# Kernel tuning notes

Hardware: AMD Instinct MI355X
Metric: run time of the kernel (lower is better)

## Reference

```python
import jax, jax.numpy as jnp
import numpy as np

EPS = 1e-3
D_MODEL = 512
SEQ = 1024
BATCH = 4
N_LAYERS = 2
N_HEAD = 8
D_HEAD = 64
D_INNER = 1024


def _position_table(n_pos, d):
    # Faithful to PositionEncoding: sin applied to even cols; the cos line in
    # the source is a no-op (missing assignment), so odd cols stay raw.
    j = np.arange(d)
    pos = np.arange(n_pos)[:, None]
    pe = pos / np.power(10000.0, 2 * (j // 2) / d)
    pe[0] = 0.0
    pe[1:, 0::2] = np.sin(pe[1:, 0::2])
    return jnp.asarray(pe, dtype=jnp.float32)


def _layer_norm(z, a, b):
    # torch.std is unbiased (ddof=1); eps added to sigma, not variance
    mu = jnp.mean(z, axis=-1, keepdims=True)
    sigma = jnp.sqrt(jnp.sum((z - mu) ** 2, axis=-1, keepdims=True) / (z.shape[-1] - 1))
    return (z - mu) / (sigma + EPS) * a + b


def setup_inputs() -> dict:
    key = jax.random.key(0)
    ks = jax.random.split(key, 10)
    s = 0.02
    return {
        "x": jax.random.normal(ks[0], (BATCH, SEQ, D_MODEL), dtype=jnp.float32),
        "pos_enc": _position_table(SEQ, D_MODEL),
        "w_qs": jax.random.normal(ks[1], (N_LAYERS, N_HEAD, D_MODEL, D_HEAD), dtype=jnp.float32) * s,
        "w_ks": jax.random.normal(ks[2], (N_LAYERS, N_HEAD, D_MODEL, D_HEAD), dtype=jnp.float32) * s,
        "w_vs": jax.random.normal(ks[3], (N_LAYERS, N_HEAD, D_MODEL, D_HEAD), dtype=jnp.float32) * s,
        "ln1_a": jnp.ones((N_LAYERS, D_MODEL), dtype=jnp.float32),
        "ln1_b": jnp.zeros((N_LAYERS, D_MODEL), dtype=jnp.float32),
        "w1": jax.random.normal(ks[4], (N_LAYERS, D_INNER, D_MODEL), dtype=jnp.float32) * s,
        "b1": jax.random.normal(ks[5], (N_LAYERS, D_INNER), dtype=jnp.float32) * s,
        "w2": jax.random.normal(ks[6], (N_LAYERS, D_MODEL, D_INNER), dtype=jnp.float32) * s,
        "b2": jax.random.normal(ks[7], (N_LAYERS, D_MODEL), dtype=jnp.float32) * s,
        "ln2_a": jnp.ones((N_LAYERS, D_MODEL), dtype=jnp.float32),
        "ln2_b": jnp.zeros((N_LAYERS, D_MODEL), dtype=jnp.float32),
    }


def reference(x, pos_enc, w_qs, w_ks, w_vs, ln1_a, ln1_b, w1, b1, w2, b2, ln2_a, ln2_b):
    temper = jnp.sqrt(jnp.float32(D_MODEL))  # scale uses d_model, not d_k (as in source)
    x = x + pos_enc[None, :, :]
    for i in range(N_LAYERS):
        residual = x
        # per-head projections: [h, b, l, dk]
        q = jnp.einsum('bld,hdk->hblk', x, w_qs[i])
        k = jnp.einsum('bld,hdk->hblk', x, w_ks[i])
        v = jnp.einsum('bld,hdv->hblv', x, w_vs[i])
        attn = jax.nn.softmax(jnp.einsum('hbqk,hbmk->hbqm', q, k) / temper, axis=-1)
        out = jnp.einsum('hbqm,hbmv->hbqv', attn, v)
        # permute(1,2,0,3): concat heads along feature dim -> [b, l, h*dv]
        out = out.transpose(1, 2, 0, 3).reshape(BATCH, SEQ, N_HEAD * D_HEAD)
        x = _layer_norm(out + residual, ln1_a[i], ln1_b[i])
        # positionwise FFN (1x1 convs == linears)
        h = jax.nn.relu(jnp.einsum('bld,fd->blf', x, w1[i]) + b1[i])
        o = jnp.einsum('blf,df->bld', h, w2[i]) + b2[i]
        x = _layer_norm(o + x, ln2_a[i], ln2_b[i])
    return x
```

## Files before the change

kernel.cpp:

```cpp
#include <hip/hip_runtime.h>
#include <math.h>

#define D_MODEL 512
#define SEQ     1024
#define BATCH   4
#define N_LAYERS 2
#define N_HEAD  8
#define D_HEAD  64
#define D_INNER 1024
#define NTOK    (BATCH*SEQ)
#define LN_EPS  1e-3f

typedef float f32x4 __attribute__((ext_vector_type(4)));
typedef short bf16x8 __attribute__((ext_vector_type(8)));
typedef unsigned short ushort_t;
typedef unsigned int uint_t;
typedef unsigned long long ull_t;

__device__ inline ushort_t f2bf(float f) {
    uint_t u = __float_as_uint(f);
    u += 0x7FFFu + ((u >> 16) & 1u);
    return (ushort_t)(u >> 16);
}
__device__ inline float bf2f(ushort_t h) {
    return __uint_as_float((uint_t)h << 16);
}

__device__ __forceinline__ void gload16(const ushort_t* g, ushort_t* l) {
    __builtin_amdgcn_global_load_lds(
        (const __attribute__((address_space(1))) void*)g,
        (__attribute__((address_space(3))) void*)l, 16, 0, 0);
}

#define PREP_E0 (NTOK * D_MODEL)
#define PREP_E1 (1536 * 512)
#define PREP_EW (N_LAYERS * D_INNER * D_MODEL)
#define PREP_TOTAL (PREP_E0 + 2 * PREP_E1 + 2 * PREP_EW)

__global__ void prep_kernel(const float* __restrict__ x,
                            const float* __restrict__ pe,
                            const float* __restrict__ w_qs,
                            const float* __restrict__ w_ks,
                            const float* __restrict__ w_vs,
                            const float* __restrict__ w1,
                            const float* __restrict__ w2,
                            float* __restrict__ X,
                            ushort_t* __restrict__ Xraw,
                            ushort_t* __restrict__ Wqkv,
                            ushort_t* __restrict__ WqkvL,
                            ushort_t* __restrict__ W1b,
                            ushort_t* __restrict__ W2b) {
    int idx = blockIdx.x * 256 + threadIdx.x;
    if (idx < PREP_E0) {
        int l = (idx / D_MODEL) % SEQ;
        int d = idx % D_MODEL;
        float xv = x[idx];
        X[idx] = xv + pe[l * D_MODEL + d];
        Xraw[idx] = f2bf(xv);
        return;
    }
    idx -= PREP_E0;
    if (idx < 2 * PREP_E1) {
        int layer = idx / PREP_E1;
        int j = idx - layer * PREP_E1;
        int n = j >> 9, k = j & 511;
        int which = n >> 9, h = (n >> 6) & 7, d = n & 63;
        size_t wofs = (size_t)layer * N_HEAD * D_MODEL * D_HEAD;
        const float* W = (which == 0) ? w_qs + wofs
                       : (which == 1) ? w_ks + wofs : w_vs + wofs;
        float v = W[((size_t)h * D_MODEL + k) * D_HEAD + d];
        ushort_t hv = f2bf(v);
        Wqkv[(size_t)layer * PREP_E1 + j] = hv;
        if (layer == 0) WqkvL[j] = f2bf(v - bf2f(hv));
        return;
    }
    idx -= 2 * PREP_E1;
    if (idx < PREP_EW) { W1b[idx] = f2bf(w1[idx]); return; }
    idx -= PREP_EW;
    W2b[idx] = f2bf(w2[idx]);
}

__device__ inline void qkv_scatter(f32x4 a, int n, int m_base,
                                   const float* __restrict__ pew,
                                   ushort_t* Qhi, ushort_t* Qlo,
                                   ushort_t* Khi, ushort_t* Klo,
                                   ushort_t* Vt) {
    int which = n >> 9, hd = n & 511;
    int head = hd >> 6, d = hd & 63;
    int hb = head * BATCH + (m_base >> 10);
    int l  = m_base & 1023;
    if (pew) {
#pragma unroll
        for (int r = 0; r < 4; r++) a[r] += pew[(size_t)(l + r) * 1536 + n];
    }
    if (which == 2) {
        ushort4 pk = make_ushort4(f2bf(a[0]), f2bf(a[1]), f2bf(a[2]), f2bf(a[3]));
        *(ushort4*)(Vt + ((size_t)hb * D_HEAD + d) * SEQ + l) = pk;
    } else {
        ushort_t* H = (which == 0) ? Qhi : Khi;
        ushort_t* L = (which == 0) ? Qlo : Klo;
#pragma unroll
        for (int r = 0; r < 4; r++) {
            float v = a[r];
            ushort_t hv = f2bf(v);
            size_t off = ((size_t)hb * SEQ + l + r) * D_HEAD + d;
            H[off] = hv;
            L[off] = f2bf(v - bf2f(hv));
        }
    }
}

template<int MODE, int TM, int TN>
__global__ __launch_bounds__(256, (TM == 128 ? 3 : 4))
void gemm_kernel(const ushort_t* __restrict__ A, const ushort_t* __restrict__ Bt,
                 const float* __restrict__ bias, const float* __restrict__ pew,
                 float* __restrict__ outF, ushort_t* __restrict__ outB,
                 ushort_t* __restrict__ Qhi, ushort_t* __restrict__ Qlo,
                 ushort_t* __restrict__ Khi, ushort_t* __restrict__ Klo,
                 ushort_t* __restrict__ Vt,
                 int M, int N, int K) {
    constexpr int BK = 128;
    constexpr int WM = TM / 2, WN = TN / 2;
    constexpr int MT = WM / 16, NT = WN / 16;
    constexpr int WA = TM / 16;
    constexpr int WB = TN / 16;
    __shared__ ushort_t As[TM * BK];
    __shared__ ushort_t Bs[TN * BK];
    const int tid = threadIdx.x;
    const int m0 = blockIdx.y * TM, n0 = blockIdx.x * TN;
    const int w = tid >> 6, lane = tid & 63;
    const int wr = w >> 1, wc = w & 1;
    const int col = lane & 15, quad = lane >> 4;
    const int srow = lane >> 4;
    const int scc  = lane & 15;

    f32x4 acc[MT][NT] = {};

    for (int k0 = 0; k0 < K; k0 += BK) {
        __syncthreads();
#pragma unroll
        for (int q = 0; q < WA; q++) {
            int row = (w * WA + q) * 4 + srow;
            int sch = scc ^ (row & 7);
            gload16(A + (size_t)(m0 + row) * K + k0 + sch * 8,
                    &As[(w * WA + q) * 4 * BK]);
        }
#pragma unroll
        for (int q = 0; q < WB; q++) {
            int row = (w * WB + q) * 4 + srow;
            int sch = scc ^ (row & 7);
            gload16(Bt + (size_t)(n0 + row) * K + k0 + sch * 8,
                    &Bs[(w * WB + q) * 4 * BK]);
        }
        __syncthreads();
#pragma unroll
        for (int ks = 0; ks < BK; ks += 32) {
            const int cb = ks >> 3;
            const int sc_ = ((cb + quad) ^ (col & 7)) * 8;
            bf16x8 af[MT], bfr[NT];
#pragma unroll
            for (int t = 0; t < MT; t++)
                af[t] = *(const bf16x8*)(&As[(wr * WM + t * 16 + col) * BK + sc_]);
#pragma unroll
            for (int t = 0; t < NT; t++)
                bfr[t] = *(const bf16x8*)(&Bs[(wc * WN + t * 16 + col) * BK + sc_]);
#pragma unroll
            for (int mt = 0; mt < MT; mt++)
#pragma unroll
                for (int nt = 0; nt < NT; nt++)
                    acc[mt][nt] = __builtin_amdgcn_mfma_f32_16x16x32_bf16(
                        af[mt], bfr[nt], acc[mt][nt], 0, 0, 0);
        }
    }

#pragma unroll
    for (int mt = 0; mt < MT; mt++) {
#pragma unroll
        for (int nt = 0; nt < NT; nt++) {
            int n = n0 + wc * WN + nt * 16 + col;
            int m_base = m0 + wr * WM + mt * 16 + quad * 4;
            if (MODE == 0) {
                qkv_scatter(acc[mt][nt], n, m_base, pew, Qhi, Qlo, Khi, Klo, Vt);
            } else {
#pragma unroll
                for (int r = 0; r < 4; r++) {
                    int m = m_base + r;
                    float v = acc[mt][nt][r];
                    if (MODE == 1) {
                        float t = fmaxf(v + bias[n], 0.f);
                        outB[(size_t)m * N + n] = f2bf(t);
                    } else {
                        outF[(size_t)m * N + n] = v + bias[n];
                    }
                }
            }
        }
    }
}

__global__ __launch_bounds__(256, 4)
void gemm_hilo_kernel(const float* __restrict__ A,
                      const ushort_t* __restrict__ Bh,
                      const ushort_t* __restrict__ Bl,
                      float* __restrict__ outF, int M, int N, int K) {
    __shared__ ushort_t Ash[64][72];
    __shared__ ushort_t Asl[64][72];
    __shared__ ushort_t Bsh[64][72];
    __shared__ ushort_t Bsl[64][72];
    const int tid = threadIdx.x;
    const int m0 = blockIdx.y * 64, n0 = blockIdx.x * 64;
    const int w = tid >> 6, lane = tid & 63;
    const int wm = (w >> 1) * 32, wn = (w & 1) * 32;
    const int col = lane & 15, quad = lane >> 4;

    f32x4 acc[2][2] = {};

    for (int k0 = 0; k0 < K; k0 += 64) {
        __syncthreads();
#pragma unroll
        for (int p = 0; p < 4; p++) {
            int idx = p * 256 + tid;
            int row = idx >> 4, c4 = (idx & 15) * 4;
            float4 v = *(const float4*)(A + (size_t)(m0 + row) * K + k0 + c4);
            ushort_t h0 = f2bf(v.x), h1 = f2bf(v.y), h2 = f2bf(v.z), h3 = f2bf(v.w);
            *(ushort4*)(&Ash[row][c4]) = make_ushort4(h0, h1, h2, h3);
            *(ushort4*)(&Asl[row][c4]) = make_ushort4(
                f2bf(v.x - bf2f(h0)), f2bf(v.y - bf2f(h1)),
                f2bf(v.z - bf2f(h2)), f2bf(v.w - bf2f(h3)));
        }
#pragma unroll
        for (int p = 0; p < 2; p++) {
            int idx = p * 256 + tid;
            int row = idx >> 3, ch = (idx & 7) * 8;
            *(uint4*)(&Bsh[row][ch]) =
                *(const uint4*)(Bh + (size_t)(n0 + row) * K + k0 + ch);
            *(uint4*)(&Bsl[row][ch]) =
                *(const uint4*)(Bl + (size_t)(n0 + row) * K + k0 + ch);
        }
        __syncthreads();
#pragma unroll
        for (int ks = 0; ks < 64; ks += 32) {
            bf16x8 ah[2], al[2], bh[2], bl[2];
#pragma unroll
            for (int t = 0; t < 2; t++) {
                ah[t] = *(const bf16x8*)(&Ash[wm + t * 16 + col][ks + quad * 8]);
                al[t] = *(const bf16x8*)(&Asl[wm + t * 16 + col][ks + quad * 8]);
                bh[t] = *(const bf16x8*)(&Bsh[wn + t * 16 + col][ks + quad * 8]);
                bl[t] = *(const bf16x8*)(&Bsl[wn + t * 16 + col][ks + quad * 8]);
            }
#pragma unroll
            for (int mt = 0; mt < 2; mt++)
#pragma unroll
                for (int nt = 0; nt < 2; nt++) {
                    acc[mt][nt] = __builtin_amdgcn_mfma_f32_16x16x32_bf16(
                        ah[mt], bh[nt], acc[mt][nt], 0, 0, 0);
                    acc[mt][nt] = __builtin_amdgcn_mfma_f32_16x16x32_bf16(
                        ah[mt], bl[nt], acc[mt][nt], 0, 0, 0);
                    acc[mt][nt] = __builtin_amdgcn_mfma_f32_16x16x32_bf16(
                        al[mt], bh[nt], acc[mt][nt], 0, 0, 0);
                }
        }
    }

#pragma unroll
    for (int mt = 0; mt < 2; mt++)
#pragma unroll
        for (int nt = 0; nt < 2; nt++) {
            int n = n0 + wn + nt * 16 + col;
#pragma unroll
            for (int r = 0; r < 4; r++) {
                int m = m0 + wm + mt * 16 + quad * 4 + r;
                outF[(size_t)m * N + n] = acc[mt][nt][r];
            }
        }
}

template<bool HILO>
__global__ __launch_bounds__(256, 2)
void attention_kernel(const ushort_t* __restrict__ Qhi,
                      const ushort_t* __restrict__ Qlo,
                      const ushort_t* __restrict__ Khi,
                      const ushort_t* __restrict__ Klo,
                      const ushort_t* __restrict__ Vt,
                      float* __restrict__ P0,
                      float* __restrict__ P1,
                      float2* __restrict__ ML) {
    const int bid = blockIdx.x;
    const int split = bid >> 8;
    const int r8  = bid & 255;
    const int j   = r8 >> 3;
    const int hb  = (r8 & 7) * 4 + (j >> 3);
    const int qp2 = j & 7;
    const int h = hb >> 2, b = hb & 3;
    const int tid = threadIdx.x;
    const int w = tid >> 6, lane = tid & 63;
    const int col = lane & 15, quad = lane >> 4;
    const size_t kbase = (size_t)hb * SEQ * D_HEAD;
    const size_t vbase = (size_t)hb * D_HEAD * SEQ;

    __shared__ ushort_t Kh[64][72];
    __shared__ ushort_t Kl[HILO ? 64 : 1][72];
    __shared__ ushort_t Vs[64][72];
    __shared__ ushort_t Pl[4][2][16][72];

    const int srow0 = tid >> 3;
    const int srow1 = 32 + (tid >> 3);
    const int sch   = (tid & 7) * 8;

    const int qbase = qp2 * 128 + w * 32;
    bf16x8 qh[2][2], ql[2][2];
#pragma unroll
    for (int u = 0; u < 2; u++) {
        const ushort_t* qp = Qhi + kbase + (size_t)(qbase + u * 16 + col) * D_HEAD;
        qh[u][0] = *(const bf16x8*)(qp + quad * 8);
        qh[u][1] = *(const bf16x8*)(qp + 32 + quad * 8);
        if (HILO) {
            const ushort_t* lp = Qlo + kbase + (size_t)(qbase + u * 16 + col) * D_HEAD;
            ql[u][0] = *(const bf16x8*)(lp + quad * 8);
            ql[u][1] = *(const bf16x8*)(lp + 32 + quad * 8);
        }
    }

    f32x4 acco[2][4] = {};
    float mrun[2] = {-1e30f, -1e30f}, lrun[2] = {0.f, 0.f};
    const float inv_temper = 0.04419417382415922f;

    const int tbeg = split * (SEQ / 2);
    const int tend = tbeg + SEQ / 2;

    uint4 rK0, rK1, rL0, rL1, rV0, rV1;
    {
        const int t0 = tbeg;
        rK0 = *(const uint4*)(Khi + kbase + (size_t)(t0 + srow0) * D_HEAD + sch);
        rK1 = *(const uint4*)(Khi + kbase + (size_t)(t0 + srow1) * D_HEAD + sch);
        if (HILO) {
            rL0 = *(const uint4*)(Klo + kbase + (size_t)(t0 + srow0) * D_HEAD + sch);
            rL1 = *(const uint4*)(Klo + kbase + (size_t)(t0 + srow1) * D_HEAD + sch);
        }
        rV0 = *(const uint4*)(Vt + vbase + (size_t)srow0 * SEQ + t0 + sch);
        rV1 = *(const uint4*)(Vt + vbase + (size_t)srow1 * SEQ + t0 + sch);
    }

    for (int t0 = tbeg; t0 < tend; t0 += 64) {
        __syncthreads();
        *(uint4*)(&Kh[srow0][sch]) = rK0;
        *(uint4*)(&Kh[srow1][sch]) = rK1;
        if (HILO) {
            *(uint4*)(&Kl[srow0][sch]) = rL0;
            *(uint4*)(&Kl[srow1][sch]) = rL1;
        }
        *(uint4*)(&Vs[srow0][sch]) = rV0;
        *(uint4*)(&Vs[srow1][sch]) = rV1;
        __syncthreads();

        if (t0 + 64 < tend) {
            const int tn = t0 + 64;
            rK0 = *(const uint4*)(Khi + kbase + (size_t)(tn + srow0) * D_HEAD + sch);
            rK1 = *(const uint4*)(Khi + kbase + (size_t)(tn + srow1) * D_HEAD + sch);
            if (HILO) {
                rL0 = *(const uint4*)(Klo + kbase + (size_t)(tn + srow0) * D_HEAD + sch);
                rL1 = *(const uint4*)(Klo + kbase + (size_t)(tn + srow1) * D_HEAD + sch);
            }
            rV0 = *(const uint4*)(Vt + vbase + (size_t)srow0 * SEQ + tn + sch);
            rV1 = *(const uint4*)(Vt + vbase + (size_t)srow1 * SEQ + tn + sch);
        }

        float sc[2][4][4];
#pragma unroll
        for (int nt = 0; nt < 4; nt++) {
            bf16x8 kh0 = *(const bf16x8*)(&Kh[nt * 16 + col][quad * 8]);
            bf16x8 kh1 = *(const bf16x8*)(&Kh[nt * 16 + col][32 + quad * 8]);
            f32x4 s0 = {}, s1 = {};
            s0 = __builtin_amdgcn_mfma_f32_16x16x32_bf16(kh0, qh[0][0], s0, 0, 0, 0);
            s0 = __builtin_amdgcn_mfma_f32_16x16x32_bf16(kh1, qh[0][1], s0, 0, 0, 0);
            s1 = __builtin_amdgcn_mfma_f32_16x16x32_bf16(kh0, qh[1][0], s1, 0, 0, 0);
            s1 = __builtin_amdgcn_mfma_f32_16x16x32_bf16(kh1, qh[1][1], s1, 0, 0, 0);
            if (HILO) {
                bf16x8 kl0 = *(const bf16x8*)(&Kl[nt * 16 + col][quad * 8]);
                bf16x8 kl1 = *(const bf16x8*)(&Kl[nt * 16 + col][32 + quad * 8]);
                s0 = __builtin_amdgcn_mfma_f32_16x16x32_bf16(kl0, qh[0][0], s0, 0, 0, 0);
                s0 = __builtin_amdgcn_mfma_f32_16x16x32_bf16(kl1, qh[0][1], s0, 0, 0, 0);
                s0 = __builtin_amdgcn_mfma_f32_16x16x32_bf16(kh0, ql[0][0], s0, 0, 0, 0);
                s0 = __builtin_amdgcn_mfma_f32_16x16x32_bf16(kh1, ql[0][1], s0, 0, 0, 0);
                s1 = __builtin_amdgcn_mfma_f32_16x16x32_bf16(kl0, qh[1][0], s1, 0, 0, 0);
                s1 = __builtin_amdgcn_mfma_f32_16x16x32_bf16(kl1, qh[1][1], s1, 0, 0, 0);
                s1 = __builtin_amdgcn_mfma_f32_16x16x32_bf16(kh0, ql[1][0], s1, 0, 0, 0);
                s1 = __builtin_amdgcn_mfma_f32_16x16x32_bf16(kh1, ql[1][1], s1, 0, 0, 0);
            }
#pragma unroll
            for (int r = 0; r < 4; r++) {
                sc[0][nt][r] = s0[r] * inv_temper;
                sc[1][nt][r] = s1[r] * inv_temper;
            }
        }

#pragma unroll
        for (int u = 0; u < 2; u++) {
            float tmax = sc[u][0][0];
#pragma unroll
            for (int nt = 0; nt < 4; nt++)
#pragma unroll
                for (int r = 0; r < 4; r++) tmax = fmaxf(tmax, sc[u][nt][r]);
            tmax = fmaxf(tmax, __shfl_xor(tmax, 16, 64));
            tmax = fmaxf(tmax, __shfl_xor(tmax, 32, 64));

            float mn = fmaxf(mrun[u], tmax);
            float alpha = __expf(mrun[u] - mn);
            mrun[u] = mn;
            float tsum = 0.f;
#pragma unroll
            for (int nt = 0; nt < 4; nt++) {
                float p0 = __expf(sc[u][nt][0] - mn);
                float p1 = __expf(sc[u][nt][1] - mn);
                float p2 = __expf(sc[u][nt][2] - mn);
                float p3 = __expf(sc[u][nt][3] - mn);
                tsum += (p0 + p1) + (p2 + p3);
                ull_t pk = (ull_t)f2bf(p0) | ((ull_t)f2bf(p1) << 16)
                         | ((ull_t)f2bf(p2) << 32) | ((ull_t)f2bf(p3) << 48);
                *(ull_t*)(&Pl[w][u][col][nt * 16 + quad * 4]) = pk;
            }
            tsum += __shfl_xor(tsum, 16, 64);
            tsum += __shfl_xor(tsum, 32, 64);
            lrun[u] = lrun[u] * alpha + tsum;
#pragma unroll
            for (int nt = 0; nt < 4; nt++)
#pragma unroll
                for (int r = 0; r < 4; r++) acco[u][nt][r] *= alpha;
        }

        __threadfence_block();

        union { ulong2 uu; bf16x8 v; } pa[2][2];
#pragma unroll
        for (int u = 0; u < 2; u++) {
            pa[u][0].uu = *(const ulong2*)(&Pl[w][u][col][quad * 8]);
            pa[u][1].uu = *(const ulong2*)(&Pl[w][u][col][32 + quad * 8]);
        }
#pragma unroll
        for (int nt = 0; nt < 4; nt++) {
            bf16x8 bv0 = *(const bf16x8*)(&Vs[nt * 16 + col][quad * 8]);
            bf16x8 bv1 = *(const bf16x8*)(&Vs[nt * 16 + col][32 + quad * 8]);
            acco[0][nt] = __builtin_amdgcn_mfma_f32_16x16x32_bf16(bv0, pa[0][0].v, acco[0][nt], 0, 0, 0);
            acco[0][nt] = __builtin_amdgcn_mfma_f32_16x16x32_bf16(bv1, pa[0][1].v, acco[0][nt], 0, 0, 0);
            acco[1][nt] = __builtin_amdgcn_mfma_f32_16x16x32_bf16(bv0, pa[1][0].v, acco[1][nt], 0, 0, 0);
            acco[1][nt] = __builtin_amdgcn_mfma_f32_16x16x32_bf16(bv1, pa[1][1].v, acco[1][nt], 0, 0, 0);
        }
    }

    float* dst = split ? P1 : P0;
#pragma unroll
    for (int u = 0; u < 2; u++) {
        const int qrow = qbase + u * 16 + col;
#pragma unroll
        for (int nt = 0; nt < 4; nt++)
            *(f32x4*)(&dst[((size_t)b * SEQ + qrow) * D_MODEL + h * D_HEAD
                           + nt * 16 + quad * 4]) = acco[u][nt];
        if (quad == 0)
            ML[((size_t)split * 32 + hb) * SEQ + qrow] = make_float2(mrun[u], lrun[u]);
    }
}

__device__ inline float block_sum_256(float v, float* tmp) {
#pragma unroll
    for (int off = 32; off > 0; off >>= 1) v += __shfl_down(v, off, 64);
    if ((threadIdx.x & 63) == 0) tmp[threadIdx.x >> 6] = v;
    __syncthreads();
    return tmp[0] + tmp[1] + tmp[2] + tmp[3];
}

__global__ void add_norm_kernel(const float* __restrict__ A,
                                const float* __restrict__ R,
                                const float* __restrict__ ga,
                                const float* __restrict__ gb,
                                float* __restrict__ Out,
                                ushort_t* __restrict__ OutBf) {
    int tok = blockIdx.x, tid = threadIdx.x;
    __shared__ float t1[4], t2[4];
    size_t base = (size_t)tok * D_MODEL;
    float z0 = A[base + tid]       + R[base + tid];
    float z1 = A[base + tid + 256] + R[base + tid + 256];
    float s = block_sum_256(z0 + z1, t1);
    float mu = s * (1.f / (float)D_MODEL);
    float d0 = z0 - mu, d1 = z1 - mu;
    float ss = block_sum_256(d0 * d0 + d1 * d1, t2);
    float sigma = sqrtf(ss * (1.f / (float)(D_MODEL - 1)));
    float inv = 1.f / (sigma + LN_EPS);
    float r0 = d0 * inv * ga[tid]       + gb[tid];
    float r1 = d1 * inv * ga[tid + 256] + gb[tid + 256];
    Out[base + tid]         = r0;
    Out[base + tid + 256]   = r1;
    OutBf[base + tid]       = f2bf(r0);
    OutBf[base + tid + 256] = f2bf(r1);
}

__global__ void add_norm_combine_kernel(const float* __restrict__ Pa,
                                        const float* __restrict__ Pb,
                                        const float2* __restrict__ ML,
                                        const float* __restrict__ R,
                                        const float* __restrict__ ga,
                                        const float* __restrict__ gb,
                                        float* __restrict__ Out,
                                        ushort_t* __restrict__ OutBf) {
    int tok = blockIdx.x, tid = threadIdx.x;
    int b = tok >> 10, l = tok & 1023;
    __shared__ float t1[4], t2[4];
    int h0 = tid >> 6;
    float s0a, s0b, s1a, s1b;
    {
        int hb0 = h0 * 4 + b;
        float2 u0 = ML[(size_t)hb0 * SEQ + l];
        float2 u1 = ML[(size_t)(32 + hb0) * SEQ + l];
        float M = fmaxf(u0.x, u1.x);
        float e0 = __expf(u0.x - M), e1 = __expf(u1.x - M);
        float inv = 1.f / (e0 * u0.y + e1 * u1.y);
        s0a = e0 * inv; s0b = e1 * inv;
        int hb1 = (h0 + 4) * 4 + b;
        float2 v0 = ML[(size_t)hb1 * SEQ + l];
        float2 v1 = ML[(size_t)(32 + hb1) * SEQ + l];
        float M2 = fmaxf(v0.x, v1.x);
        float f0 = __expf(v0.x - M2), f1 = __expf(v1.x - M2);
        float inv2 = 1.f / (f0 * v0.y + f1 * v1.y);
        s1a = f0 * inv2; s1b = f1 * inv2;
    }
    size_t base = (size_t)tok * D_MODEL;
    float z0 = Pa[base + tid] * s0a + Pb[base + tid] * s0b + R[base + tid];
    float z1 = Pa[base + tid + 256] * s1a + Pb[base + tid + 256] * s1b
             + R[base + tid + 256];
    float s = block_sum_256(z0 + z1, t1);
    float mu = s * (1.f / (float)D_MODEL);
    float d0 = z0 - mu, d1 = z1 - mu;
    float ss = block_sum_256(d0 * d0 + d1 * d1, t2);
    float sigma = sqrtf(ss * (1.f / (float)(D_MODEL - 1)));
    float inv = 1.f / (sigma + LN_EPS);
    float r0 = d0 * inv * ga[tid]       + gb[tid];
    float r1 = d1 * inv * ga[tid + 256] + gb[tid + 256];
    Out[base + tid]         = r0;
    Out[base + tid + 256]   = r1;
    OutBf[base + tid]       = f2bf(r0);
    OutBf[base + tid + 256] = f2bf(r1);
}

extern "C" void kernel_launch(void* const* d_in, const int* in_sizes, int n_in,
                              void* d_out, int out_size, void* d_ws, size_t ws_size,
                              hipStream_t stream) {
    const float* x     = (const float*)d_in[0];
    const float* pe    = (const float*)d_in[1];
    const float* w_qs  = (const float*)d_in[2];
    const float* w_ks  = (const float*)d_in[3];
    const float* w_vs  = (const float*)d_in[4];
    const float* ln1_a = (const float*)d_in[5];
    const float* ln1_b = (const float*)d_in[6];
    const float* w1    = (const float*)d_in[7];
    const float* b1    = (const float*)d_in[8];
    const float* w2    = (const float*)d_in[9];
    const float* b2    = (const float*)d_in[10];
    const float* ln2_a = (const float*)d_in[11];
    const float* ln2_b = (const float*)d_in[12];
    float* out = (float*)d_out;

    const size_t NXD = (size_t)NTOK * D_MODEL;
    char* p = (char*)d_ws;
    float*    X    = (float*)p;     p += NXD * 4;
    float*    Ob   = (float*)p;     p += NXD * 4;
    ushort_t* Xbf  = (ushort_t*)p;  p += NXD * 2;
    ushort_t* Xraw = (ushort_t*)p;  p += NXD * 2;
    ushort_t* Qhi  = (ushort_t*)p;  p += NXD * 2;
    ushort_t* Qlo  = (ushort_t*)p;  p += NXD * 2;
    ushort_t* Khi  = (ushort_t*)p;  p += NXD * 2;
    ushort_t* Klo  = (ushort_t*)p;  p += NXD * 2;
    ushort_t* Vt   = (ushort_t*)p;  p += NXD * 2;
    ushort_t* Wqkv = (ushort_t*)p;  p += (size_t)N_LAYERS * 1536 * 512 * 2;
    ushort_t* WqkvL= (ushort_t*)p;  p += (size_t)1536 * 512 * 2;
    ushort_t* W1b  = (ushort_t*)p;  p += (size_t)N_LAYERS * D_INNER * D_MODEL * 2;
    ushort_t* W2b  = (ushort_t*)p;  p += (size_t)N_LAYERS * D_MODEL * D_INNER * 2;
    float2*   ML   = (float2*)p;
    ushort_t* Hbf  = Qhi;
    float*    PEW  = Ob;

    prep_kernel<<<(PREP_TOTAL + 255) / 256, 256, 0, stream>>>(
        x, pe, w_qs, w_ks, w_vs, w1, w2, X, Xraw, Wqkv, WqkvL, W1b, W2b);

    for (int i = 0; i < N_LAYERS; i++) {
        if (i == 0) {
            gemm_hilo_kernel<<<dim3(1536 / 64, SEQ / 64), 256, 0, stream>>>(
                pe, Wqkv, WqkvL, PEW, SEQ, 1536, D_MODEL);
            gemm_kernel<0, 128, 64><<<dim3(1536 / 64, NTOK / 128), 256, 0, stream>>>(
                Xraw, Wqkv, nullptr, PEW, nullptr, nullptr,
                Qhi, Qlo, Khi, Klo, Vt, NTOK, 1536, D_MODEL);
            attention_kernel<true><<<512, 256, 0, stream>>>(
                Qhi, Qlo, Khi, Klo, Vt, Ob, out, ML);
        } else {
            gemm_kernel<0, 128, 64><<<dim3(1536 / 64, NTOK / 128), 256, 0, stream>>>(
                Xbf, Wqkv + (size_t)i * 1536 * 512, nullptr, nullptr, nullptr,
                nullptr, Qhi, Qlo, Khi, Klo, Vt, NTOK, 1536, D_MODEL);
            attention_kernel<false><<<512, 256, 0, stream>>>(
                Qhi, Qlo, Khi, Klo, Vt, Ob, out, ML);
        }

        add_norm_combine_kernel<<<NTOK, 256, 0, stream>>>(
            Ob, out, ML, X, ln1_a + i * D_MODEL, ln1_b + i * D_MODEL, X, Xbf);

        gemm_kernel<1, 128, 64><<<dim3(D_INNER / 64, NTOK / 128), 256, 0, stream>>>(
            Xbf, W1b + (size_t)i * D_INNER * D_MODEL, b1 + (size_t)i * D_INNER,
            nullptr, nullptr, Hbf, nullptr, nullptr, nullptr, nullptr, nullptr,
            NTOK, D_INNER, D_MODEL);

        gemm_kernel<2, 64, 64><<<dim3(D_MODEL / 64, NTOK / 64), 256, 0, stream>>>(
            Hbf, W2b + (size_t)i * D_MODEL * D_INNER, b2 + (size_t)i * D_MODEL,
            nullptr, Ob, nullptr, nullptr, nullptr, nullptr, nullptr, nullptr,
            NTOK, D_MODEL, D_INNER);

        float* dst = (i == N_LAYERS - 1) ? out : X;
        add_norm_kernel<<<NTOK, 256, 0, stream>>>(
            Ob, X, ln2_a + i * D_MODEL, ln2_b + i * D_MODEL, dst, Xbf);
    }
}
```

Baseline: 271.9 us.

## Double-buffer attention K/V tiles and use one wave per token in layernorm

The attention kernel now keeps two LDS buffers for K, K-lo and V. The next tile is written into the spare buffer after the PV MFMAs, which removes one __syncthreads per iteration and lets global prefetch overlap compute. In exchange, LDS use per block roughly doubles, which may cut occupancy. The two add+layernorm kernels now map one 64-lane wave per token with vectorized 8-element loads and shuffle-only reductions, removing shared-memory block reductions and cutting the block count by four.

```diff
diff --git a/kernel.cpp b/kernel.cpp
--- a/kernel.cpp
+++ b/kernel.cpp
@@ -298,9 +298,9 @@
     const size_t kbase = (size_t)hb * SEQ * D_HEAD;
     const size_t vbase = (size_t)hb * D_HEAD * SEQ;
 
-    __shared__ ushort_t Kh[64][72];
-    __shared__ ushort_t Kl[HILO ? 64 : 1][72];
-    __shared__ ushort_t Vs[64][72];
+    __shared__ ushort_t Kh[2][64][72];
+    __shared__ ushort_t Kl[HILO ? 2 : 1][64][72];
+    __shared__ ushort_t Vs[2][64][72];
     __shared__ ushort_t Pl[4][2][16][72];
 
     const int srow0 = tid >> 3;
@@ -339,45 +339,43 @@
         }
         rV0 = *(const uint4*)(Vt + vbase + (size_t)srow0 * SEQ + t0 + sch);
         rV1 = *(const uint4*)(Vt + vbase + (size_t)srow1 * SEQ + t0 + sch);
-    }
-
+        *(uint4*)(&Kh[0][srow0][sch]) = rK0;
+        *(uint4*)(&Kh[0][srow1][sch]) = rK1;
+        if (HILO) {
+            *(uint4*)(&Kl[0][srow0][sch]) = rL0;
+            *(uint4*)(&Kl[0][srow1][sch]) = rL1;
+        }
+        *(uint4*)(&Vs[0][srow0][sch]) = rV0;
+        *(uint4*)(&Vs[0][srow1][sch]) = rV1;
+    }
+    __syncthreads();
+    if (tbeg + 64 < tend) {
+        const int tn = tbeg + 64;
+        rK0 = *(const uint4*)(Khi + kbase + (size_t)(tn + srow0) * D_HEAD + sch);
+        rK1 = *(const uint4*)(Khi + kbase + (size_t)(tn + srow1) * D_HEAD + sch);
+        if (HILO) {
+            rL0 = *(const uint4*)(Klo + kbase + (size_t)(tn + srow0) * D_HEAD + sch);
+            rL1 = *(const uint4*)(Klo + kbase + (size_t)(tn + srow1) * D_HEAD + sch);
+        }
+        rV0 = *(const uint4*)(Vt + vbase + (size_t)srow0 * SEQ + tn + sch);
+        rV1 = *(const uint4*)(Vt + vbase + (size_t)srow1 * SEQ + tn + sch);
+    }
+
+    int cur = 0;
     for (int t0 = tbeg; t0 < tend; t0 += 64) {
-        __syncthreads();
-        *(uint4*)(&Kh[srow0][sch]) = rK0;
-        *(uint4*)(&Kh[srow1][sch]) = rK1;
-        if (HILO) {
-            *(uint4*)(&Kl[srow0][sch]) = rL0;
-            *(uint4*)(&Kl[srow1][sch]) = rL1;
-        }
-        *(uint4*)(&Vs[srow0][sch]) = rV0;
-        *(uint4*)(&Vs[srow1][sch]) = rV1;
-        __syncthreads();
-
-        if (t0 + 64 < tend) {
-            const int tn = t0 + 64;
-            rK0 = *(const uint4*)(Khi + kbase + (size_t)(tn + srow0) * D_HEAD + sch);
-            rK1 = *(const uint4*)(Khi + kbase + (size_t)(tn + srow1) * D_HEAD + sch);
-            if (HILO) {
-                rL0 = *(const uint4*)(Klo + kbase + (size_t)(tn + srow0) * D_HEAD + sch);
-                rL1 = *(const uint4*)(Klo + kbase + (size_t)(tn + srow1) * D_HEAD + sch);
-            }
-            rV0 = *(const uint4*)(Vt + vbase + (size_t)srow0 * SEQ + tn + sch);
-            rV1 = *(const uint4*)(Vt + vbase + (size_t)srow1 * SEQ + tn + sch);
-        }
-
         float sc[2][4][4];
 #pragma unroll
         for (int nt = 0; nt < 4; nt++) {
-            bf16x8 kh0 = *(const bf16x8*)(&Kh[nt * 16 + col][quad * 8]);
-            bf16x8 kh1 = *(const bf16x8*)(&Kh[nt * 16 + col][32 + quad * 8]);
+            bf16x8 kh0 = *(const bf16x8*)(&Kh[cur][nt * 16 + col][quad * 8]);
+            bf16x8 kh1 = *(const bf16x8*)(&Kh[cur][nt * 16 + col][32 + quad * 8]);
             f32x4 s0 = {}, s1 = {};
             s0 = __builtin_amdgcn_mfma_f32_16x16x32_bf16(kh0, qh[0][0], s0, 0, 0, 0);
             s0 = __builtin_amdgcn_mfma_f32_16x16x32_bf16(kh1, qh[0][1], s0, 0, 0, 0);
             s1 = __builtin_amdgcn_mfma_f32_16x16x32_bf16(kh0, qh[1][0], s1, 0, 0, 0);
             s1 = __builtin_amdgcn_mfma_f32_16x16x32_bf16(kh1, qh[1][1], s1, 0, 0, 0);
             if (HILO) {
-                bf16x8 kl0 = *(const bf16x8*)(&Kl[nt * 16 + col][quad * 8]);
-                bf16x8 kl1 = *(const bf16x8*)(&Kl[nt * 16 + col][32 + quad * 8]);
+                bf16x8 kl0 = *(const bf16x8*)(&Kl[cur][nt * 16 + col][quad * 8]);
+                bf16x8 kl1 = *(const bf16x8*)(&Kl[cur][nt * 16 + col][32 + quad * 8]);
                 s0 = __builtin_amdgcn_mfma_f32_16x16x32_bf16(kl0, qh[0][0], s0, 0, 0, 0);
                 s0 = __builtin_amdgcn_mfma_f32_16x16x32_bf16(kl1, qh[0][1], s0, 0, 0, 0);
                 s0 = __builtin_amdgcn_mfma_f32_16x16x32_bf16(kh0, ql[0][0], s0, 0, 0, 0);
@@ -438,13 +436,37 @@
         }
 #pragma unroll
         for (int nt = 0; nt < 4; nt++) {
-            bf16x8 bv0 = *(const bf16x8*)(&Vs[nt * 16 + col][quad * 8]);
-            bf16x8 bv1 = *(const bf16x8*)(&Vs[nt * 16 + col][32 + quad * 8]);
+            bf16x8 bv0 = *(const bf16x8*)(&Vs[cur][nt * 16 + col][quad * 8]);
+            bf16x8 bv1 = *(const bf16x8*)(&Vs[cur][nt * 16 + col][32 + quad * 8]);
             acco[0][nt] = __builtin_amdgcn_mfma_f32_16x16x32_bf16(bv0, pa[0][0].v, acco[0][nt], 0, 0, 0);
             acco[0][nt] = __builtin_amdgcn_mfma_f32_16x16x32_bf16(bv1, pa[0][1].v, acco[0][nt], 0, 0, 0);
             acco[1][nt] = __builtin_amdgcn_mfma_f32_16x16x32_bf16(bv0, pa[1][0].v, acco[1][nt], 0, 0, 0);
             acco[1][nt] = __builtin_amdgcn_mfma_f32_16x16x32_bf16(bv1, pa[1][1].v, acco[1][nt], 0, 0, 0);
         }
+
+        if (t0 + 64 < tend) {
+            *(uint4*)(&Kh[cur ^ 1][srow0][sch]) = rK0;
+            *(uint4*)(&Kh[cur ^ 1][srow1][sch]) = rK1;
+            if (HILO) {
+                *(uint4*)(&Kl[cur ^ 1][srow0][sch]) = rL0;
+                *(uint4*)(&Kl[cur ^ 1][srow1][sch]) = rL1;
+            }
+            *(uint4*)(&Vs[cur ^ 1][srow0][sch]) = rV0;
+            *(uint4*)(&Vs[cur ^ 1][srow1][sch]) = rV1;
+            if (t0 + 128 < tend) {
+                const int tn = t0 + 128;
+                rK0 = *(const uint4*)(Khi + kbase + (size_t)(tn + srow0) * D_HEAD + sch);
+                rK1 = *(const uint4*)(Khi + kbase + (size_t)(tn + srow1) * D_HEAD + sch);
+                if (HILO) {
+                    rL0 = *(const uint4*)(Klo + kbase + (size_t)(tn + srow0) * D_HEAD + sch);
+                    rL1 = *(const uint4*)(Klo + kbase + (size_t)(tn + srow1) * D_HEAD + sch);
+                }
+                rV0 = *(const uint4*)(Vt + vbase + (size_t)srow0 * SEQ + tn + sch);
+                rV1 = *(const uint4*)(Vt + vbase + (size_t)srow1 * SEQ + tn + sch);
+            }
+        }
+        __syncthreads();
+        cur ^= 1;
     }
 
     float* dst = split ? P1 : P0;
@@ -460,12 +482,10 @@
     }
 }
 
-__device__ inline float block_sum_256(float v, float* tmp) {
-#pragma unroll
-    for (int off = 32; off > 0; off >>= 1) v += __shfl_down(v, off, 64);
-    if ((threadIdx.x & 63) == 0) tmp[threadIdx.x >> 6] = v;
-    __syncthreads();
-    return tmp[0] + tmp[1] + tmp[2] + tmp[3];
+__device__ __forceinline__ float wave_sum_64(float v) {
+#pragma unroll
+    for (int off = 32; off > 0; off >>= 1) v += __shfl_xor(v, off, 64);
+    return v;
 }
 
 __global__ void add_norm_kernel(const float* __restrict__ A,
@@ -474,23 +494,44 @@
                                 const float* __restrict__ gb,
                                 float* __restrict__ Out,
                                 ushort_t* __restrict__ OutBf) {
-    int tok = blockIdx.x, tid = threadIdx.x;
-    __shared__ float t1[4], t2[4];
-    size_t base = (size_t)tok * D_MODEL;
-    float z0 = A[base + tid]       + R[base + tid];
-    float z1 = A[base + tid + 256] + R[base + tid + 256];
-    float s = block_sum_256(z0 + z1, t1);
+    int tok = blockIdx.x * 4 + (threadIdx.x >> 6);
+    int lane = threadIdx.x & 63;
+    size_t base = (size_t)tok * D_MODEL + lane * 8;
+    f32x4 a0 = *(const f32x4*)(A + base);
+    f32x4 a1 = *(const f32x4*)(A + base + 4);
+    f32x4 r0 = *(const f32x4*)(R + base);
+    f32x4 r1 = *(const f32x4*)(R + base + 4);
+    f32x4 z0, z1;
+#pragma unroll
+    for (int t = 0; t < 4; t++) { z0[t] = a0[t] + r0[t]; z1[t] = a1[t] + r1[t]; }
+    float s = (z0[0] + z0[1] + z0[2] + z0[3]) + (z1[0] + z1[1] + z1[2] + z1[3]);
+    s = wave_sum_64(s);
     float mu = s * (1.f / (float)D_MODEL);
-    float d0 = z0 - mu, d1 = z1 - mu;
-    float ss = block_sum_256(d0 * d0 + d1 * d1, t2);
+    float ss = 0.f;
+#pragma unroll
+    for (int t = 0; t < 4; t++) {
+        float d0 = z0[t] - mu, d1 = z1[t] - mu;
+        ss += d0 * d0 + d1 * d1;
+    }
+    ss = wave_sum_64(ss);
     float sigma = sqrtf(ss * (1.f / (float)(D_MODEL - 1)));
     float inv = 1.f / (sigma + LN_EPS);
-    float r0 = d0 * inv * ga[tid]       + gb[tid];
-    float r1 = d1 * inv * ga[tid + 256] + gb[tid + 256];
-    Out[base + tid]         = r0;
-    Out[base + tid + 256]   = r1;
-    OutBf[base + tid]       = f2bf(r0);
-    OutBf[base + tid + 256] = f2bf(r1);
+    f32x4 g0 = *(const f32x4*)(ga + lane * 8);
+    f32x4 g1 = *(const f32x4*)(ga + lane * 8 + 4);
+    f32x4 h0 = *(const f32x4*)(gb + lane * 8);
+    f32x4 h1 = *(const f32x4*)(gb + lane * 8 + 4);
+    f32x4 o0, o1;
+    bf16x8 pk;
+#pragma unroll
+    for (int t = 0; t < 4; t++) {
+        o0[t] = (z0[t] - mu) * inv * g0[t] + h0[t];
+        o1[t] = (z1[t] - mu) * inv * g1[t] + h1[t];
+        pk[t] = (short)f2bf(o0[t]);
+        pk[t + 4] = (short)f2bf(o1[t]);
+    }
+    *(f32x4*)(Out + base) = o0;
+    *(f32x4*)(Out + base + 4) = o1;
+    *(bf16x8*)(OutBf + base) = pk;
 }
 
 __global__ void add_norm_combine_kernel(const float* __restrict__ Pa,
@@ -501,43 +542,57 @@
                                         const float* __restrict__ gb,
                                         float* __restrict__ Out,
                                         ushort_t* __restrict__ OutBf) {
-    int tok = blockIdx.x, tid = threadIdx.x;
+    int tok = blockIdx.x * 4 + (threadIdx.x >> 6);
+    int lane = threadIdx.x & 63;
     int b = tok >> 10, l = tok & 1023;
-    __shared__ float t1[4], t2[4];
-    int h0 = tid >> 6;
-    float s0a, s0b, s1a, s1b;
-    {
-        int hb0 = h0 * 4 + b;
-        float2 u0 = ML[(size_t)hb0 * SEQ + l];
-        float2 u1 = ML[(size_t)(32 + hb0) * SEQ + l];
-        float M = fmaxf(u0.x, u1.x);
-        float e0 = __expf(u0.x - M), e1 = __expf(u1.x - M);
-        float inv = 1.f / (e0 * u0.y + e1 * u1.y);
-        s0a = e0 * inv; s0b = e1 * inv;
-        int hb1 = (h0 + 4) * 4 + b;
-        float2 v0 = ML[(size_t)hb1 * SEQ + l];
-        float2 v1 = ML[(size_t)(32 + hb1) * SEQ + l];
-        float M2 = fmaxf(v0.x, v1.x);
-        float f0 = __expf(v0.x - M2), f1 = __expf(v1.x - M2);
-        float inv2 = 1.f / (f0 * v0.y + f1 * v1.y);
-        s1a = f0 * inv2; s1b = f1 * inv2;
-    }
-    size_t base = (size_t)tok * D_MODEL;
-    float z0 = Pa[base + tid] * s0a + Pb[base + tid] * s0b + R[base + tid];
-    float z1 = Pa[base + tid + 256] * s1a + Pb[base + tid + 256] * s1b
-             + R[base + tid + 256];
-    float s = block_sum_256(z0 + z1, t1);
+    int hb0 = (lane >> 3) * 4 + b;
+    float2 u0 = ML[(size_t)hb0 * SEQ + l];
+    float2 u1 = ML[(size_t)(32 + hb0) * SEQ + l];
+    float M = fmaxf(u0.x, u1.x);
+    float e0 = __expf(u0.x - M), e1 = __expf(u1.x - M);
+    float sinv = 1.f / (e0 * u0.y + e1 * u1.y);
+    float sa = e0 * sinv, sb = e1 * sinv;
+    size_t base = (size_t)tok * D_MODEL + lane * 8;
+    f32x4 pa0 = *(const f32x4*)(Pa + base);
+    f32x4 pa1 = *(const f32x4*)(Pa + base + 4);
+    f32x4 pb0 = *(const f32x4*)(Pb + base);
+    f32x4 pb1 = *(const f32x4*)(Pb + base + 4);
+    f32x4 r0 = *(const f32x4*)(R + base);
+    f32x4 r1 = *(const f32x4*)(R + base + 4);
+    f32x4 z0, z1;
+#pragma unroll
+    for (int t = 0; t < 4; t++) {
+        z0[t] = pa0[t] * sa + pb0[t] * sb + r0[t];
+        z1[t] = pa1[t] * sa + pb1[t] * sb + r1[t];
+    }
+    float s = (z0[0] + z0[1] + z0[2] + z0[3]) + (z1[0] + z1[1] + z1[2] + z1[3]);
+    s = wave_sum_64(s);
     float mu = s * (1.f / (float)D_MODEL);
-    float d0 = z0 - mu, d1 = z1 - mu;
-    float ss = block_sum_256(d0 * d0 + d1 * d1, t2);
+    float ss = 0.f;
+#pragma unroll
+    for (int t = 0; t < 4; t++) {
+        float d0 = z0[t] - mu, d1 = z1[t] - mu;
+        ss += d0 * d0 + d1 * d1;
+    }
+    ss = wave_sum_64(ss);
     float sigma = sqrtf(ss * (1.f / (float)(D_MODEL - 1)));
     float inv = 1.f / (sigma + LN_EPS);
-    float r0 = d0 * inv * ga[tid]       + gb[tid];
-    float r1 = d1 * inv * ga[tid + 256] + gb[tid + 256];
-    Out[base + tid]         = r0;
-    Out[base + tid + 256]   = r1;
-    OutBf[base + tid]       = f2bf(r0);
-    OutBf[base + tid + 256] = f2bf(r1);
+    f32x4 g0 = *(const f32x4*)(ga + lane * 8);
+    f32x4 g1 = *(const f32x4*)(ga + lane * 8 + 4);
+    f32x4 h0 = *(const f32x4*)(gb + lane * 8);
+    f32x4 h1 = *(const f32x4*)(gb + lane * 8 + 4);
+    f32x4 o0, o1;
+    bf16x8 pk;
+#pragma unroll
+    for (int t = 0; t < 4; t++) {
+        o0[t] = (z0[t] - mu) * inv * g0[t] + h0[t];
+        o1[t] = (z1[t] - mu) * inv * g1[t] + h1[t];
+        pk[t] = (short)f2bf(o0[t]);
+        pk[t + 4] = (short)f2bf(o1[t]);
+    }
+    *(f32x4*)(Out + base) = o0;
+    *(f32x4*)(Out + base + 4) = o1;
+    *(bf16x8*)(OutBf + base) = pk;
 }
 
 extern "C" void kernel_launch(void* const* d_in, const int* in_sizes, int n_in,
@@ -597,7 +652,7 @@
                 Qhi, Qlo, Khi, Klo, Vt, Ob, out, ML);
         }
 
-        add_norm_combine_kernel<<<NTOK, 256, 0, stream>>>(
+        add_norm_combine_kernel<<<NTOK / 4, 256, 0, stream>>>(
             Ob, out, ML, X, ln1_a + i * D_MODEL, ln1_b + i * D_MODEL, X, Xbf);
 
         gemm_kernel<1, 128, 64><<<dim3(D_INNER / 64, NTOK / 128), 256, 0, stream>>>(
@@ -611,7 +666,7 @@
             NTOK, D_MODEL, D_INNER);
 
         float* dst = (i == N_LAYERS - 1) ? out : X;
-        add_norm_kernel<<<NTOK, 256, 0, stream>>>(
+        add_norm_kernel<<<NTOK / 4, 256, 0, stream>>>(
             Ob, X, ln2_a + i * D_MODEL, ln2_b + i * D_MODEL, dst, Xbf);
     }
 }
```

New measurement: 268.1 us. Within noise of the previous version (-1.4%).
